# Performance work log

Hardware: AMD Instinct MI355X
Metric: run time of the kernel (lower is better)

Reference implementation:

```python
import jax, jax.numpy as jnp
import numpy as np
import math

D_MODEL = 1024
N_HEADS = 16
HEAD_DIM = D_MODEL // N_HEADS
BATCH = 2
SEQ = 4096


def setup_inputs() -> dict:
    key = jax.random.key(0)
    ks = jax.random.split(key, 12)
    s = 0.02
    inp = {
        "query": jax.random.normal(ks[0], (BATCH, SEQ, D_MODEL), jnp.float32),
        "key": jax.random.normal(ks[1], (BATCH, SEQ, D_MODEL), jnp.float32),
        "value": jax.random.normal(ks[2], (BATCH, SEQ, D_MODEL), jnp.float32),
        "mask": jnp.ones((1, 1, SEQ, SEQ), jnp.int32),
        "Wq": jax.random.normal(ks[3], (D_MODEL, D_MODEL), jnp.float32) * s,
        "bq": jax.random.normal(ks[4], (D_MODEL,), jnp.float32) * s,
        "Wk": jax.random.normal(ks[5], (D_MODEL, D_MODEL), jnp.float32) * s,
        "bk": jax.random.normal(ks[6], (D_MODEL,), jnp.float32) * s,
        "Wv": jax.random.normal(ks[7], (D_MODEL, D_MODEL), jnp.float32) * s,
        "bv": jax.random.normal(ks[8], (D_MODEL,), jnp.float32) * s,
        "Wo": jax.random.normal(ks[9], (D_MODEL, D_MODEL), jnp.float32) * s,
        "bo": jax.random.normal(ks[10], (D_MODEL,), jnp.float32) * s,
    }
    return inp


def reference(query, key, value, mask, Wq, bq, Wk, bk, Wv, bv, Wo, bo):
    B, S, D = query.shape
    scale = 1.0 / math.sqrt(HEAD_DIM)

    def proj_split(x, W, b):
        # Linear (torch convention x @ W.T + b) then split heads -> [B, H, S, Dh]
        y = x @ W.T + b
        return y.reshape(B, -1, N_HEADS, HEAD_DIM).transpose(0, 2, 1, 3)

    q = proj_split(query, Wq, bq)
    k = proj_split(key, Wk, bk)
    v = proj_split(value, Wv, bv)

    # naive materialized scores [B, H, Sq, Sk]
    scores = jnp.einsum("bhqd,bhkd->bhqk", q, k) * scale
    scores = jnp.where(mask == 0, jnp.float32(-1e9), scores)
    probs = jax.nn.softmax(scores, axis=-1)
    attn = jnp.einsum("bhqk,bhkd->bhqd", probs, v)

    # combine heads -> [B, S, D]
    out = attn.transpose(0, 2, 1, 3).reshape(B, S, D)
    return out @ Wo.T + bo
```

## Files before the change

kernel.cpp:

```cpp
#include <hip/hip_runtime.h>

typedef float f32x4  __attribute__((ext_vector_type(4)));
typedef float f32x16 __attribute__((ext_vector_type(16)));
typedef __bf16 bf16x8 __attribute__((ext_vector_type(8)));
typedef unsigned u32x2 __attribute__((ext_vector_type(2)));
typedef unsigned u32x4 __attribute__((ext_vector_type(4)));

#define DEV static __device__ __forceinline__

constexpr int SEQ_ = 4096;
constexpr int DM_  = 1024;
constexpr int NH_  = 16;
constexpr int DH_  = 64;

DEV unsigned short f2bf(float f) {
    union { float f; unsigned u; } v; v.f = f;
    return (unsigned short)((v.u + 0x7fffu + ((v.u >> 16) & 1u)) >> 16);
}

DEV unsigned cvtpk_bf16(float lo, float hi) {
    unsigned r;
    asm("v_cvt_pk_bf16_f32 %0, %1, %2" : "=v"(r) : "v"(lo), "v"(hi));
    return r;
}

DEV void gll16(const void* g, void* l) {
    __builtin_amdgcn_global_load_lds(
        (const __attribute__((address_space(1))) void*)g,
        (__attribute__((address_space(3))) void*)l,
        16, 0, 0);
}

__global__ void cast_f32_bf16(const float* __restrict__ in,
                              unsigned short* __restrict__ out, int n4) {
    int i = blockIdx.x * blockDim.x + threadIdx.x;
    if (i < n4) {
        float4 v = ((const float4*)in)[i];
        ushort4 o;
        o.x = f2bf(v.x); o.y = f2bf(v.y); o.z = f2bf(v.z); o.w = f2bf(v.w);
        ((ushort4*)out)[i] = o;
    }
}

template<int MODE>
__global__ __launch_bounds__(256, 2)
void gemm_bt(const unsigned short* __restrict__ A,
             const unsigned short* __restrict__ Bw,
             const float* __restrict__ bias,
             void* __restrict__ Cout,
             int M, int N, int K)
{
    __shared__ char As[128 * 128];
    __shared__ char Bs[128 * 128];

    const int tid = threadIdx.x;
    const int w = tid >> 6, lane = tid & 63;
    const int wr = w >> 1, wc = w & 1;
    const int lr = lane & 15, lg = lane >> 4;

    const int nwg = gridDim.x * gridDim.y;
    const int bid = blockIdx.y * gridDim.x + blockIdx.x;
    const int id  = (bid & 7) * (nwg >> 3) + (bid >> 3);
    const int bx = id & 7;
    const int by = id >> 3;
    const int m0 = by * 128, n0 = bx * 128;

    f32x4 acc[4][4] = {};

    for (int kt = 0; kt < K / 64; ++kt) {
        const int k0 = kt * 64;
        __syncthreads();
        #pragma unroll
        for (int i = 0; i < 4; ++i) {
            int ch = w * 4 + i;
            int o = (ch * 64 + lane) * 16;
            int row = o >> 7, cb = o & 127;
            int cbs = cb ^ ((row & 7) << 4);
            gll16((const char*)A  + ((size_t)(m0 + row) * K + k0) * 2 + cbs, As + ch * 1024);
            gll16((const char*)Bw + ((size_t)(n0 + row) * K + k0) * 2 + cbs, Bs + ch * 1024);
        }
        __syncthreads();

        #pragma unroll
        for (int kf = 0; kf < 2; ++kf) {
            bf16x8 af[4], bfv[4];
            #pragma unroll
            for (int mf = 0; mf < 4; ++mf) {
                int row = wr * 64 + mf * 16 + lr;
                int cb = (kf * 64 + lg * 16) ^ ((row & 7) << 4);
                af[mf] = *(const bf16x8*)(As + row * 128 + cb);
            }
            #pragma unroll
            for (int nf = 0; nf < 4; ++nf) {
                int row = wc * 64 + nf * 16 + lr;
                int cb = (kf * 64 + lg * 16) ^ ((row & 7) << 4);
                bfv[nf] = *(const bf16x8*)(Bs + row * 128 + cb);
            }
            #pragma unroll
            for (int mf = 0; mf < 4; ++mf)
                #pragma unroll
                for (int nf = 0; nf < 4; ++nf)
                    acc[mf][nf] = __builtin_amdgcn_mfma_f32_16x16x32_bf16(
                        af[mf], bfv[nf], acc[mf][nf], 0, 0, 0);
        }
    }

    #pragma unroll
    for (int nf = 0; nf < 4; ++nf) {
        int gn = n0 + wc * 64 + nf * 16 + lr;
        float bv = bias[gn];
        #pragma unroll
        for (int mf = 0; mf < 4; ++mf) {
            #pragma unroll
            for (int r = 0; r < 4; ++r) {
                int gm = m0 + wr * 64 + mf * 16 + lg * 4 + r;
                float val = acc[mf][nf][r] + bv;
                if (MODE == 1) {
                    ((float*)Cout)[(size_t)gm * N + gn] = val;
                } else {
                    int b = gm >> 12, s = gm & (SEQ_ - 1);
                    int h = gn >> 6, dh = gn & (DH_ - 1);
                    size_t idx = (MODE == 0)
                        ? (((size_t)(b * NH_ + h) * SEQ_ + s) * DH_ + dh)
                        : (((size_t)(b * NH_ + h) * DH_ + dh) * SEQ_ + s);
                    ((unsigned short*)Cout)[idx] = f2bf(val);
                }
            }
        }
    }
}

__global__ __launch_bounds__(256, 3)
void attn_fwd(const unsigned short* __restrict__ Qb,
              const unsigned short* __restrict__ Kb,
              const unsigned short* __restrict__ Vtb,
              unsigned short* __restrict__ ctx)
{
    __shared__ char Ks[2][64 * 128];
    __shared__ char Vs[2][64 * 128];

    const int tid = threadIdx.x;
    const int w = tid >> 6, lane = tid & 63;
    const int l31 = lane & 31, hi = lane >> 5;

    const int nwg = gridDim.x * gridDim.y;
    const int bid = blockIdx.y * gridDim.x + blockIdx.x;
    const int id  = (bid & 7) * (nwg >> 3) + (bid >> 3);
    const int qt = id & 31;
    const int bh = id >> 5;

    const unsigned short* Qh = Qb  + (size_t)bh * SEQ_ * DH_;
    const unsigned short* Kh = Kb  + (size_t)bh * SEQ_ * DH_;
    const unsigned short* Vh = Vtb + (size_t)bh * DH_ * SEQ_;
    const int q0 = qt * 128 + w * 32;
    const int q  = q0 + l31;

    bf16x8 qa[4];
    #pragma unroll
    for (int kk = 0; kk < 4; ++kk)
        qa[kk] = *(const bf16x8*)(Qh + (size_t)q * DH_ + kk * 16 + hi * 8);

    float m_run = -1e30f, l_run = 0.f;
    f32x16 o_acc[2] = {};
    constexpr float CEXP = 0.125f * 1.44269504088896340736f;

    auto stage = [&](int buf, int kv0) {
        #pragma unroll
        for (int i = 0; i < 2; ++i) {
            int ch = w * 2 + i;
            int o = (ch * 64 + lane) * 16;
            int row = o >> 7, cb = o & 127;
            int cbs = cb ^ ((row & 7) << 4);
            gll16((const char*)Kh + ((size_t)(kv0 + row) * DH_) * 2 + cbs, Ks[buf] + ch * 1024);
            gll16((const char*)Vh + ((size_t)row * SEQ_ + kv0) * 2 + cbs, Vs[buf] + ch * 1024);
        }
    };

    int cur = 0;
    stage(0, 0);

    for (int kt = 0; kt < SEQ_ / 64; ++kt) {
        __syncthreads();
        if (kt + 1 < SEQ_ / 64) stage(cur ^ 1, (kt + 1) * 64);

        const char* Ksb = Ks[cur];
        const char* Vsb = Vs[cur];

        f32x16 sacc[2] = {};
        __builtin_amdgcn_s_setprio(1);
        #pragma unroll
        for (int kk = 0; kk < 4; ++kk) {
            #pragma unroll
            for (int sub = 0; sub < 2; ++sub) {
                int krow = sub * 32 + l31;
                bf16x8 kf = *(const bf16x8*)(Ksb + krow * 128 +
                                ((32 * kk + 16 * hi) ^ ((krow & 7) << 4)));
                sacc[sub] = __builtin_amdgcn_mfma_f32_32x32x16_bf16(kf, qa[kk], sacc[sub], 0, 0, 0);
            }
        }
        __builtin_amdgcn_s_setprio(0);

        float mloc = -1e30f;
        #pragma unroll
        for (int sub = 0; sub < 2; ++sub)
            #pragma unroll
            for (int r = 0; r < 16; ++r) mloc = fmaxf(mloc, sacc[sub][r]);
        float mfull = fmaxf(mloc, __shfl_xor(mloc, 32));

        if (!__all(mfull - m_run <= 64.f)) {
            float mnew = fmaxf(m_run, mfull);
            float corr = __builtin_amdgcn_exp2f((m_run - mnew) * CEXP);
            l_run *= corr;
            #pragma unroll
            for (int d = 0; d < 2; ++d) o_acc[d] *= corr;
            m_run = mnew;
        }

        float pv[2][16];
        float rs = 0.f;
        #pragma unroll
        for (int sub = 0; sub < 2; ++sub)
            #pragma unroll
            for (int r = 0; r < 16; ++r) {
                float p = __builtin_amdgcn_exp2f((sacc[sub][r] - m_run) * CEXP);
                pv[sub][r] = p; rs += p;
            }
        rs += __shfl_xor(rs, 32);
        l_run += rs;

        unsigned c0[8], c1[8];
        #pragma unroll
        for (int g = 0; g < 8; ++g) {
            int sub = g >> 2, u = g & 3;
            c0[g] = cvtpk_bf16(pv[sub][4 * u + 0], pv[sub][4 * u + 1]);
            c1[g] = cvtpk_bf16(pv[sub][4 * u + 2], pv[sub][4 * u + 3]);
        }

        __builtin_amdgcn_s_setprio(1);
        #pragma unroll
        for (int ks = 0; ks < 4; ++ks) {
            u32x2 s0 = __builtin_amdgcn_permlane32_swap(c0[2 * ks], c0[2 * ks + 1], false, false);
            u32x2 s1 = __builtin_amdgcn_permlane32_swap(c1[2 * ks], c1[2 * ks + 1], false, false);
            u32x4 pw; pw[0] = s0[0]; pw[1] = s1[0]; pw[2] = s0[1]; pw[3] = s1[1];
            bf16x8 pfrag = __builtin_bit_cast(bf16x8, pw);
            #pragma unroll
            for (int dsub = 0; dsub < 2; ++dsub) {
                int vrow = dsub * 32 + l31;
                bf16x8 vf = *(const bf16x8*)(Vsb + vrow * 128 +
                                ((32 * ks + 16 * hi) ^ ((vrow & 7) << 4)));
                o_acc[dsub] = __builtin_amdgcn_mfma_f32_32x32x16_bf16(vf, pfrag, o_acc[dsub], 0, 0, 0);
            }
        }
        __builtin_amdgcn_s_setprio(0);

        cur ^= 1;
    }

    const int b = bh >> 4, h = bh & 15;
    const float inv = 1.f / l_run;
    unsigned short* orow = ctx + ((size_t)(b * SEQ_ + q)) * DM_ + h * 64;
    #pragma unroll
    for (int dsub = 0; dsub < 2; ++dsub)
        #pragma unroll
        for (int u = 0; u < 4; ++u) {
            ushort4 o4;
            o4.x = f2bf(o_acc[dsub][4 * u + 0] * inv);
            o4.y = f2bf(o_acc[dsub][4 * u + 1] * inv);
            o4.z = f2bf(o_acc[dsub][4 * u + 2] * inv);
            o4.w = f2bf(o_acc[dsub][4 * u + 3] * inv);
            *(ushort4*)(orow + dsub * 32 + 8 * u + 4 * hi) = o4;
        }
}

extern "C" void kernel_launch(void* const* d_in, const int* in_sizes, int n_in,
                              void* d_out, int out_size, void* d_ws, size_t ws_size,
                              hipStream_t stream)
{
    const float* q_in = (const float*)d_in[0];
    const float* k_in = (const float*)d_in[1];
    const float* v_in = (const float*)d_in[2];
    const float* Wq = (const float*)d_in[4];
    const float* bq = (const float*)d_in[5];
    const float* Wk = (const float*)d_in[6];
    const float* bk = (const float*)d_in[7];
    const float* Wv = (const float*)d_in[8];
    const float* bv = (const float*)d_in[9];
    const float* Wo = (const float*)d_in[10];
    const float* bo = (const float*)d_in[11];

    char* ws = (char*)d_ws;
    const size_t MB16 = (size_t)2 * SEQ_ * DM_ * 2;
    const size_t WSZ  = (size_t)DM_ * DM_ * 2;

    unsigned short* Xq  = (unsigned short*)(ws);
    unsigned short* Xk  = (unsigned short*)(ws + MB16);
    unsigned short* Xv  = (unsigned short*)(ws + 2 * MB16);
    unsigned short* Wqb = (unsigned short*)(ws + 3 * MB16);
    unsigned short* Wkb = (unsigned short*)(ws + 3 * MB16 + WSZ);
    unsigned short* Wvb = (unsigned short*)(ws + 3 * MB16 + 2 * WSZ);
    unsigned short* Wob = (unsigned short*)(ws + 3 * MB16 + 3 * WSZ);
    unsigned short* Qb  = (unsigned short*)(ws + 3 * MB16 + 4 * WSZ);
    unsigned short* Kb  = (unsigned short*)(ws + 4 * MB16 + 4 * WSZ);
    unsigned short* Vt  = (unsigned short*)(ws + 5 * MB16 + 4 * WSZ);
    unsigned short* Ctx = Xq;

    const int nx = 2 * SEQ_ * DM_;
    const int nw = DM_ * DM_;
    cast_f32_bf16<<<(nx / 4 + 255) / 256, 256, 0, stream>>>(q_in, Xq, nx / 4);
    cast_f32_bf16<<<(nx / 4 + 255) / 256, 256, 0, stream>>>(k_in, Xk, nx / 4);
    cast_f32_bf16<<<(nx / 4 + 255) / 256, 256, 0, stream>>>(v_in, Xv, nx / 4);
    cast_f32_bf16<<<(nw / 4 + 255) / 256, 256, 0, stream>>>(Wq, Wqb, nw / 4);
    cast_f32_bf16<<<(nw / 4 + 255) / 256, 256, 0, stream>>>(Wk, Wkb, nw / 4);
    cast_f32_bf16<<<(nw / 4 + 255) / 256, 256, 0, stream>>>(Wv, Wvb, nw / 4);
    cast_f32_bf16<<<(nw / 4 + 255) / 256, 256, 0, stream>>>(Wo, Wob, nw / 4);

    dim3 gg(DM_ / 128, 2 * SEQ_ / 128);
    gemm_bt<0><<<gg, 256, 0, stream>>>(Xq, Wqb, bq, Qb, 2 * SEQ_, DM_, DM_);
    gemm_bt<0><<<gg, 256, 0, stream>>>(Xk, Wkb, bk, Kb, 2 * SEQ_, DM_, DM_);
    gemm_bt<2><<<gg, 256, 0, stream>>>(Xv, Wvb, bv, Vt, 2 * SEQ_, DM_, DM_);

    attn_fwd<<<dim3(32, 32), 256, 0, stream>>>(Qb, Kb, Vt, Ctx);

    gemm_bt<1><<<gg, 256, 0, stream>>>(Ctx, Wob, bo, d_out, 2 * SEQ_, DM_, DM_);
}
```

Measured before the change: 309.8 us.

## Fold softmax scale into Q projection and use 512-thread attention blocks

The softmax scale and log2e factor are now applied in the Q projection epilogue, which removes a multiply per score inside the attention loop. The attention kernel moves from 256 to 512 threads per block, covering 256 queries with 8 waves that share each K/V tile, so each wave stages one chunk instead of two. The exp and bf16 pack loops are fused and the max reduction is restructured, and the lazy-rescale threshold is retuned for log2-domain scores. Risks are the Q rounding to bf16 after scaling, and fewer grid blocks (512) with higher per-block resource needs under launch bounds of (512,4).

Result: faster. 292.0 us (-5.7%).

```diff
diff --git a/kernel.cpp b/kernel.cpp
--- a/kernel.cpp
+++ b/kernel.cpp
@@ -48,7 +48,7 @@
              const unsigned short* __restrict__ Bw,
              const float* __restrict__ bias,
              void* __restrict__ Cout,
-             int M, int N, int K)
+             int M, int N, int K, float oscale)
 {
     __shared__ char As[128 * 128];
     __shared__ char Bs[128 * 128];
@@ -114,7 +114,7 @@
             #pragma unroll
             for (int r = 0; r < 4; ++r) {
                 int gm = m0 + wr * 64 + mf * 16 + lg * 4 + r;
-                float val = acc[mf][nf][r] + bv;
+                float val = (acc[mf][nf][r] + bv) * oscale;
                 if (MODE == 1) {
                     ((float*)Cout)[(size_t)gm * N + gn] = val;
                 } else {
@@ -130,7 +130,7 @@
     }
 }
 
-__global__ __launch_bounds__(256, 3)
+__global__ __launch_bounds__(512, 4)
 void attn_fwd(const unsigned short* __restrict__ Qb,
               const unsigned short* __restrict__ Kb,
               const unsigned short* __restrict__ Vtb,
@@ -146,13 +146,13 @@
     const int nwg = gridDim.x * gridDim.y;
     const int bid = blockIdx.y * gridDim.x + blockIdx.x;
     const int id  = (bid & 7) * (nwg >> 3) + (bid >> 3);
-    const int qt = id & 31;
-    const int bh = id >> 5;
+    const int qt = id & 15;
+    const int bh = id >> 4;
 
     const unsigned short* Qh = Qb  + (size_t)bh * SEQ_ * DH_;
     const unsigned short* Kh = Kb  + (size_t)bh * SEQ_ * DH_;
     const unsigned short* Vh = Vtb + (size_t)bh * DH_ * SEQ_;
-    const int q0 = qt * 128 + w * 32;
+    const int q0 = qt * 256 + w * 32;
     const int q  = q0 + l31;
 
     bf16x8 qa[4];
@@ -162,18 +162,13 @@
 
     float m_run = -1e30f, l_run = 0.f;
     f32x16 o_acc[2] = {};
-    constexpr float CEXP = 0.125f * 1.44269504088896340736f;
 
     auto stage = [&](int buf, int kv0) {
-        #pragma unroll
-        for (int i = 0; i < 2; ++i) {
-            int ch = w * 2 + i;
-            int o = (ch * 64 + lane) * 16;
-            int row = o >> 7, cb = o & 127;
-            int cbs = cb ^ ((row & 7) << 4);
-            gll16((const char*)Kh + ((size_t)(kv0 + row) * DH_) * 2 + cbs, Ks[buf] + ch * 1024);
-            gll16((const char*)Vh + ((size_t)row * SEQ_ + kv0) * 2 + cbs, Vs[buf] + ch * 1024);
-        }
+        int o = (w * 64 + lane) * 16;
+        int row = o >> 7, cb = o & 127;
+        int cbs = cb ^ ((row & 7) << 4);
+        gll16((const char*)Kh + ((size_t)(kv0 + row) * DH_) * 2 + cbs, Ks[buf] + w * 1024);
+        gll16((const char*)Vh + ((size_t)row * SEQ_ + kv0) * 2 + cbs, Vs[buf] + w * 1024);
     };
 
     int cur = 0;
@@ -202,39 +197,39 @@
 
         float mloc = -1e30f;
         #pragma unroll
-        for (int sub = 0; sub < 2; ++sub)
-            #pragma unroll
-            for (int r = 0; r < 16; ++r) mloc = fmaxf(mloc, sacc[sub][r]);
+        for (int sub = 0; sub < 2; ++sub) {
+            float a = fmaxf(fmaxf(sacc[sub][0], sacc[sub][1]), sacc[sub][2]);
+            #pragma unroll
+            for (int r = 3; r < 15; r += 2)
+                a = fmaxf(fmaxf(a, sacc[sub][r]), sacc[sub][r + 1]);
+            mloc = fmaxf(mloc, fmaxf(a, sacc[sub][15]));
+        }
         float mfull = fmaxf(mloc, __shfl_xor(mloc, 32));
 
-        if (!__all(mfull - m_run <= 64.f)) {
+        if (!__all(mfull - m_run <= 11.5f)) {
             float mnew = fmaxf(m_run, mfull);
-            float corr = __builtin_amdgcn_exp2f((m_run - mnew) * CEXP);
+            float corr = __builtin_amdgcn_exp2f(m_run - mnew);
             l_run *= corr;
             #pragma unroll
             for (int d = 0; d < 2; ++d) o_acc[d] *= corr;
             m_run = mnew;
         }
 
-        float pv[2][16];
+        unsigned c0[8], c1[8];
         float rs = 0.f;
         #pragma unroll
-        for (int sub = 0; sub < 2; ++sub)
-            #pragma unroll
-            for (int r = 0; r < 16; ++r) {
-                float p = __builtin_amdgcn_exp2f((sacc[sub][r] - m_run) * CEXP);
-                pv[sub][r] = p; rs += p;
-            }
+        for (int g = 0; g < 8; ++g) {
+            int sub = g >> 2, u = g & 3;
+            float e0 = __builtin_amdgcn_exp2f(sacc[sub][4 * u + 0] - m_run);
+            float e1 = __builtin_amdgcn_exp2f(sacc[sub][4 * u + 1] - m_run);
+            float e2 = __builtin_amdgcn_exp2f(sacc[sub][4 * u + 2] - m_run);
+            float e3 = __builtin_amdgcn_exp2f(sacc[sub][4 * u + 3] - m_run);
+            rs += (e0 + e1) + (e2 + e3);
+            c0[g] = cvtpk_bf16(e0, e1);
+            c1[g] = cvtpk_bf16(e2, e3);
+        }
         rs += __shfl_xor(rs, 32);
         l_run += rs;
-
-        unsigned c0[8], c1[8];
-        #pragma unroll
-        for (int g = 0; g < 8; ++g) {
-            int sub = g >> 2, u = g & 3;
-            c0[g] = cvtpk_bf16(pv[sub][4 * u + 0], pv[sub][4 * u + 1]);
-            c1[g] = cvtpk_bf16(pv[sub][4 * u + 2], pv[sub][4 * u + 3]);
-        }
 
         __builtin_amdgcn_s_setprio(1);
         #pragma unroll
@@ -314,12 +309,13 @@
     cast_f32_bf16<<<(nw / 4 + 255) / 256, 256, 0, stream>>>(Wv, Wvb, nw / 4);
     cast_f32_bf16<<<(nw / 4 + 255) / 256, 256, 0, stream>>>(Wo, Wob, nw / 4);
 
+    const float qscale = 0.125f * 1.44269504088896340736f;
     dim3 gg(DM_ / 128, 2 * SEQ_ / 128);
-    gemm_bt<0><<<gg, 256, 0, stream>>>(Xq, Wqb, bq, Qb, 2 * SEQ_, DM_, DM_);
-    gemm_bt<0><<<gg, 256, 0, stream>>>(Xk, Wkb, bk, Kb, 2 * SEQ_, DM_, DM_);
-    gemm_bt<2><<<gg, 256, 0, stream>>>(Xv, Wvb, bv, Vt, 2 * SEQ_, DM_, DM_);
-
-    attn_fwd<<<dim3(32, 32), 256, 0, stream>>>(Qb, Kb, Vt, Ctx);
-
-    gemm_bt<1><<<gg, 256, 0, stream>>>(Ctx, Wob, bo, d_out, 2 * SEQ_, DM_, DM_);
-}
+    gemm_bt<0><<<gg, 256, 0, stream>>>(Xq, Wqb, bq, Qb, 2 * SEQ_, DM_, DM_, qscale);
+    gemm_bt<0><<<gg, 256, 0, stream>>>(Xk, Wkb, bk, Kb, 2 * SEQ_, DM_, DM_, 1.0f);
+    gemm_bt<2><<<gg, 256, 0, stream>>>(Xv, Wvb, bv, Vt, 2 * SEQ_, DM_, DM_, 1.0f);
+
+    attn_fwd<<<dim3(16, 32), 512, 0, stream>>>(Qb, Kb, Vt, Ctx);
+
+    gemm_bt<1><<<gg, 256, 0, stream>>>(Ctx, Wob, bo, d_out, 2 * SEQ_, DM_, DM_, 1.0f);
+}
```
